# Performance work log

Hardware: AMD Instinct MI355X
Metric: run time of the kernel (lower is better)

## Reference

```python
import jax, jax.numpy as jnp
import numpy as np
import math

B, T, VOCAB, RANK = 32, 1024, 512, 256


def setup_inputs() -> dict:
    key = jax.random.key(0)
    k1, k2, k3, k4, k5 = jax.random.split(key, 5)
    scale_attn = 1.0 / math.sqrt(VOCAB)
    scale_proj = 1.0 / math.sqrt(RANK)
    return {
        "x": jax.random.normal(k1, (B, T, VOCAB), dtype=jnp.float32),
        "W_attn": jax.random.normal(k2, (VOCAB, 3 * RANK), dtype=jnp.float32) * scale_attn,
        "b_attn": jax.random.normal(k3, (3 * RANK,), dtype=jnp.float32) * 0.01,
        "W_proj": jax.random.normal(k4, (RANK, VOCAB), dtype=jnp.float32) * scale_proj,
        "b_proj": jax.random.normal(k5, (VOCAB,), dtype=jnp.float32) * 0.01,
    }


def reference(x, W_attn, b_attn, W_proj, b_proj):
    # x: [B, T, vocab]
    Bb, Tt, _ = x.shape
    qkv = x @ W_attn + b_attn              # [B, T, 3*rank]
    q, k, v = jnp.split(qkv, 3, axis=-1)   # each [B, T, rank]
    scale = 1.0 / math.sqrt(k.shape[-1])
    att = jnp.einsum('btd,bsd->bts', q, k) * scale  # [B, T, T]
    # causal mask (masked=True)
    mask = jnp.tril(jnp.ones((Tt, Tt), dtype=bool))
    att = jnp.where(mask[None, :, :], att, -jnp.inf)
    att = jax.nn.softmax(att, axis=-1)
    # dropout layers are identity in eval mode (p=0 attn, p=0.1 resid disabled)
    y = jnp.einsum('bts,bsd->btd', att, v)  # [B, T, rank]
    y = y @ W_proj + b_proj                 # [B, T, vocab]
    return jax.nn.gelu(y, approximate=False)
```

## Files before the change

### kernel.cpp

```cpp
#include <hip/hip_runtime.h>
#include <hip/hip_bf16.h>
#include <math.h>

typedef __bf16 bf16;
typedef __attribute__((ext_vector_type(8))) __bf16 bf16x8;
typedef __attribute__((ext_vector_type(4))) __bf16 bf16x4;
typedef __attribute__((ext_vector_type(4))) float f32x4;

#define MFMA16(a, b, c) __builtin_amdgcn_mfma_f32_16x16x32_bf16((a), (b), (c), 0, 0, 0)

__device__ __forceinline__ void glds16(const bf16* g, bf16* l) {
  __builtin_amdgcn_global_load_lds(
      (const __attribute__((address_space(1))) unsigned int*)g,
      (__attribute__((address_space(3))) unsigned int*)l, 16, 0, 0);
}


__global__ __launch_bounds__(256) void cvt_wattn(const float* __restrict__ w,
                                                 bf16* __restrict__ wt) {
  int o = blockIdx.x * 256 + threadIdx.x;
  int n = o >> 9, kk = o & 511;
  wt[o] = (bf16)w[kk * 768 + n];
}

__global__ __launch_bounds__(256) void cvt_wproj(const float* __restrict__ w,
                                                 bf16* __restrict__ wt) {
  int o = blockIdx.x * 256 + threadIdx.x;
  int n = o >> 8, kk = o & 255;
  wt[o] = (bf16)w[kk * 512 + n];
}

__global__ __launch_bounds__(256) void cvt_x(const float* __restrict__ x,
                                             bf16* __restrict__ xb) {
  size_t i = ((size_t)blockIdx.x * 256 + threadIdx.x) * 8;
  f32x4 f0 = *(const f32x4*)(x + i);
  f32x4 f1 = *(const f32x4*)(x + i + 4);
  bf16x8 h;
#pragma unroll
  for (int e = 0; e < 4; ++e) { h[e] = (bf16)f0[e]; h[e + 4] = (bf16)f1[e]; }
  *(bf16x8*)(xb + i) = h;
}

__global__ __launch_bounds__(256) void gemm_qkv(
    const bf16* __restrict__ xb, const bf16* __restrict__ WT,
    const float* __restrict__ b_attn,
    bf16* __restrict__ qo, bf16* __restrict__ ko, bf16* __restrict__ vo) {
  __shared__ __attribute__((aligned(16))) bf16 As[128][32];
  __shared__ __attribute__((aligned(16))) bf16 Bs[128][32];
  const int tid = threadIdx.x;
  const int id = blockIdx.x;
  const int xcd = id & 7;
  const int rest = id >> 3;
  const int bmL = rest / 6;
  const int bn = (rest % 6) * 128;
  const int bm = (xcd * 32 + bmL) * 128;
  const int lane = tid & 63, wid = tid >> 6;
  const int l15 = lane & 15, lg = lane >> 4;
  const int wm = (wid >> 1) * 64, wn = (wid & 1) * 64;

  f32x4 acc[4][4] = {};

  const int ar = tid >> 2;
  const int ac = (tid & 3) * 8;
  const bf16* aB = xb + (size_t)bm * 512 + (size_t)ar * 512 + ac;
  const bf16* bB = WT + (size_t)bn * 512 + (size_t)ar * 512 + ac;
  bf16* As0 = &As[0][0];
  bf16* Bs0 = &Bs[0][0];

  for (int kt = 0; kt < 16; ++kt) {
    const int k0 = kt * 32;
    glds16(aB + k0,            As0 + (size_t)tid * 8);
    glds16(aB + 64 * 512 + k0, As0 + (size_t)(256 + tid) * 8);
    glds16(bB + k0,            Bs0 + (size_t)tid * 8);
    glds16(bB + 64 * 512 + k0, Bs0 + (size_t)(256 + tid) * 8);
    __syncthreads();
    bf16x8 af[4], bfr[4];
#pragma unroll
    for (int mi = 0; mi < 4; ++mi)
      af[mi] = *(const bf16x8*)&As[wm + mi * 16 + l15][lg * 8];
#pragma unroll
    for (int ni = 0; ni < 4; ++ni)
      bfr[ni] = *(const bf16x8*)&Bs[wn + ni * 16 + l15][lg * 8];
#pragma unroll
    for (int mi = 0; mi < 4; ++mi)
#pragma unroll
      for (int ni = 0; ni < 4; ++ni)
        acc[mi][ni] = MFMA16(bfr[ni], af[mi], acc[mi][ni]);
    __syncthreads();
  }

#pragma unroll
  for (int ni = 0; ni < 4; ++ni) {
    int gc0 = bn + wn + ni * 16 + lg * 4;
    f32x4 bias = *(const f32x4*)(b_attn + gc0);
    int seg = gc0 >> 8;
    int cc = gc0 & 255;
    bf16* op = (seg == 0) ? qo : ((seg == 1) ? ko : vo);
#pragma unroll
    for (int mi = 0; mi < 4; ++mi) {
      int gr = bm + wm + mi * 16 + l15;
      bf16x4 pk;
#pragma unroll
      for (int r = 0; r < 4; ++r) pk[r] = (bf16)(acc[mi][ni][r] + bias[r]);
      *(bf16x4*)(op + (size_t)gr * 256 + cc) = pk;
    }
  }
}

__global__ __launch_bounds__(256) void transpose_v(const bf16* __restrict__ v,
                                                   bf16* __restrict__ vt) {
  __shared__ bf16 tile[32][33];
  const int b = blockIdx.z;
  const int t0 = blockIdx.x * 32;
  const int d0 = blockIdx.y * 32;
  const int tid = threadIdx.x;
  const int r = tid >> 3, c4 = (tid & 7) * 4;
  bf16x4 in = *(const bf16x4*)(v + (size_t)(b * 1024 + t0 + r) * 256 + d0 + c4);
  tile[r][c4] = in[0]; tile[r][c4 + 1] = in[1];
  tile[r][c4 + 2] = in[2]; tile[r][c4 + 3] = in[3];
  __syncthreads();
  bf16x4 o;
  o[0] = tile[c4][r]; o[1] = tile[c4 + 1][r];
  o[2] = tile[c4 + 2][r]; o[3] = tile[c4 + 3][r];
  *(bf16x4*)(vt + (size_t)(b * 256 + d0 + r) * 1024 + t0 + c4) = o;
}

__global__ __launch_bounds__(512) void attn_fwd(
    const bf16* __restrict__ q, const bf16* __restrict__ k,
    const bf16* __restrict__ vt, bf16* __restrict__ y) {
  __shared__ __attribute__((aligned(16))) bf16 Ks[64][264];
  __shared__ __attribute__((aligned(16))) bf16 Vt[256][72];
  __shared__ __attribute__((aligned(16))) bf16 Ps[8][16][72];
  const int tid = threadIdx.x, lane = tid & 63, wid = tid >> 6;
  const int l15 = lane & 15, lg = lane >> 4;

  const int id = blockIdx.x;
  const int xcd = id & 7;
  const int rest = id >> 3;
  const int qt = rest & 7;
  const int bg = rest >> 3;
  const int b = xcd + 8 * bg;
  const int q0 = qt * 128 + wid * 16;

  bf16x8 qf[8];
  {
    const bf16* qp = q + (size_t)(b * 1024 + q0 + l15) * 256 + lg * 8;
#pragma unroll
    for (int d = 0; d < 8; ++d) qf[d] = *(const bf16x8*)(qp + d * 32);
  }
  f32x4 o[16] = {};
  float m_st = -1e30f;
  float l_st = 0.f;

  const bf16* kbase = k + (size_t)b * 1024 * 256;
  const bf16* vtbase = vt + (size_t)b * 256 * 1024;
  const int ksr = tid >> 5, ksc = (tid & 31) * 8;
  const int vsr = tid >> 3, vsc = (tid & 7) * 8;

  const int ntiles = 2 * qt + 2;

  bf16x8 kreg[4], vreg[4];
#pragma unroll
  for (int i = 0; i < 4; ++i)
    kreg[i] = *(const bf16x8*)(kbase + (size_t)(ksr + i * 16) * 256 + ksc);
#pragma unroll
  for (int i = 0; i < 4; ++i)
    vreg[i] = *(const bf16x8*)(vtbase + (size_t)(vsr + i * 64) * 1024 + vsc);

  for (int tt = 0; tt < ntiles; ++tt) {
    const int kv0 = tt * 64;
    __syncthreads();
#pragma unroll
    for (int i = 0; i < 4; ++i)
      *(bf16x8*)&Ks[ksr + i * 16][ksc] = kreg[i];
#pragma unroll
    for (int i = 0; i < 4; ++i)
      *(bf16x8*)&Vt[vsr + i * 64][vsc] = vreg[i];
    __syncthreads();
    if (tt + 1 < ntiles) {
      const bf16* kp = kbase + (size_t)(kv0 + 64 + ksr) * 256 + ksc;
      const bf16* vp = vtbase + (size_t)vsr * 1024 + kv0 + 64 + vsc;
#pragma unroll
      for (int i = 0; i < 4; ++i)
        kreg[i] = *(const bf16x8*)(kp + (size_t)i * 16 * 256);
#pragma unroll
      for (int i = 0; i < 4; ++i)
        vreg[i] = *(const bf16x8*)(vp + (size_t)i * 64 * 1024);
    }

    f32x4 st[4] = {};
    __builtin_amdgcn_s_setprio(1);
#pragma unroll
    for (int nf = 0; nf < 4; ++nf)
#pragma unroll
      for (int dc = 0; dc < 8; ++dc) {
        bf16x8 kb = *(const bf16x8*)&Ks[nf * 16 + l15][dc * 32 + lg * 8];
        st[nf] = MFMA16(kb, qf[dc], st[nf]);
      }
    __builtin_amdgcn_s_setprio(0);

    const int qg = q0 + l15;
    float tmax = -1e30f;
#pragma unroll
    for (int nf = 0; nf < 4; ++nf)
#pragma unroll
      for (int r = 0; r < 4; ++r) {
        int sg = kv0 + nf * 16 + lg * 4 + r;
        float v = st[nf][r] * 0.0625f;
        v = (sg > qg) ? -1e30f : v;
        st[nf][r] = v;
        tmax = fmaxf(tmax, v);
      }
    tmax = fmaxf(tmax, __shfl_xor(tmax, 16, 64));
    tmax = fmaxf(tmax, __shfl_xor(tmax, 32, 64));

    if (!__all(tmax <= m_st + 8.f)) {
      float mnew = fmaxf(m_st, tmax);
      float corr = __expf(m_st - mnew);
      m_st = mnew;
      l_st *= corr;
#pragma unroll
      for (int df = 0; df < 16; ++df)
#pragma unroll
        for (int r = 0; r < 4; ++r) o[df][r] *= corr;
    }

    float rsum = 0.f;
#pragma unroll
    for (int nf = 0; nf < 4; ++nf) {
      bf16x4 pk;
#pragma unroll
      for (int r = 0; r < 4; ++r) {
        float p = __expf(st[nf][r] - m_st);
        rsum += p;
        pk[r] = (bf16)p;
      }
      *(bf16x4*)&Ps[wid][l15][nf * 16 + lg * 4] = pk;
    }
    rsum += __shfl_xor(rsum, 16, 64);
    rsum += __shfl_xor(rsum, 32, 64);
    l_st += rsum;

    bf16x8 pa0 = *(const bf16x8*)&Ps[wid][l15][lg * 8];
    bf16x8 pa1 = *(const bf16x8*)&Ps[wid][l15][32 + lg * 8];
    __builtin_amdgcn_s_setprio(1);
#pragma unroll
    for (int df = 0; df < 16; ++df) {
      bf16x8 vb0 = *(const bf16x8*)&Vt[df * 16 + l15][lg * 8];
      bf16x8 vb1 = *(const bf16x8*)&Vt[df * 16 + l15][32 + lg * 8];
      o[df] = MFMA16(vb0, pa0, o[df]);
      o[df] = MFMA16(vb1, pa1, o[df]);
    }
    __builtin_amdgcn_s_setprio(0);
  }

  float inv = 1.f / l_st;
  bf16* yp = y + (size_t)(b * 1024 + q0 + l15) * 256 + lg * 4;
#pragma unroll
  for (int df = 0; df < 16; ++df) {
    bf16x4 pk;
#pragma unroll
    for (int r = 0; r < 4; ++r) pk[r] = (bf16)(o[df][r] * inv);
    *(bf16x4*)(yp + df * 16) = pk;
  }
}

__global__ __launch_bounds__(256) void gemm_proj(
    const bf16* __restrict__ y, const bf16* __restrict__ WT,
    const float* __restrict__ b_proj, float* __restrict__ out) {
  __shared__ __attribute__((aligned(16))) bf16 As[128][32];
  __shared__ __attribute__((aligned(16))) bf16 Bs[128][32];
  const int tid = threadIdx.x;
  const int id = blockIdx.x;
  const int xcd = id & 7;
  const int rest = id >> 3;
  const int bmL = rest >> 2;
  const int bn = (rest & 3) * 128;
  const int bm = (xcd * 32 + bmL) * 128;
  const int lane = tid & 63, wid = tid >> 6;
  const int l15 = lane & 15, lg = lane >> 4;
  const int wm = (wid >> 1) * 64, wn = (wid & 1) * 64;
  f32x4 acc[4][4] = {};

  const int ar = tid >> 2;
  const int ac = (tid & 3) * 8;
  const bf16* aB = y + (size_t)bm * 256 + (size_t)ar * 256 + ac;
  const bf16* bB = WT + (size_t)bn * 256 + (size_t)ar * 256 + ac;
  bf16* As0 = &As[0][0];
  bf16* Bs0 = &Bs[0][0];

  for (int kt = 0; kt < 8; ++kt) {
    const int k0 = kt * 32;
    glds16(aB + k0,            As0 + (size_t)tid * 8);
    glds16(aB + 64 * 256 + k0, As0 + (size_t)(256 + tid) * 8);
    glds16(bB + k0,            Bs0 + (size_t)tid * 8);
    glds16(bB + 64 * 256 + k0, Bs0 + (size_t)(256 + tid) * 8);
    __syncthreads();
    bf16x8 af[4], bfr[4];
#pragma unroll
    for (int mi = 0; mi < 4; ++mi)
      af[mi] = *(const bf16x8*)&As[wm + mi * 16 + l15][lg * 8];
#pragma unroll
    for (int ni = 0; ni < 4; ++ni)
      bfr[ni] = *(const bf16x8*)&Bs[wn + ni * 16 + l15][lg * 8];
#pragma unroll
    for (int mi = 0; mi < 4; ++mi)
#pragma unroll
      for (int ni = 0; ni < 4; ++ni)
        acc[mi][ni] = MFMA16(bfr[ni], af[mi], acc[mi][ni]);
    __syncthreads();
  }

#pragma unroll
  for (int ni = 0; ni < 4; ++ni) {
    int gc0 = bn + wn + ni * 16 + lg * 4;
    f32x4 bias = *(const f32x4*)(b_proj + gc0);
#pragma unroll
    for (int mi = 0; mi < 4; ++mi) {
      int gr = bm + wm + mi * 16 + l15;
      f32x4 g;
#pragma unroll
      for (int r = 0; r < 4; ++r) {
        float v = acc[mi][ni][r] + bias[r];
        float z = 1.5957691216f * (v + 0.044715f * v * v * v);
        float t = __expf(z);
        float th = 1.f - 2.f / (t + 1.f);
        g[r] = 0.5f * v * (1.f + th);
      }
      *(f32x4*)(out + (size_t)gr * 512 + gc0) = g;
    }
  }
}

extern "C" void kernel_launch(void* const* d_in, const int* in_sizes, int n_in,
                              void* d_out, int out_size, void* d_ws, size_t ws_size,
                              hipStream_t stream) {
  const float* x      = (const float*)d_in[0];
  const float* W_attn = (const float*)d_in[1];
  const float* b_attn = (const float*)d_in[2];
  const float* W_proj = (const float*)d_in[3];
  const float* b_proj = (const float*)d_in[4];
  float* out = (float*)d_out;
  char* ws = (char*)d_ws;

  const size_t SZ = 16777216;
  bf16* WT1 = (bf16*)(ws);
  bf16* WT2 = (bf16*)(ws + 786432);
  bf16* qb  = (bf16*)(ws + 1048576);
  bf16* kb  = (bf16*)(ws + 1048576 + SZ);
  bf16* vb  = (bf16*)(ws + 1048576 + 2 * SZ);
  bf16* vtb = (bf16*)(ws + 1048576 + 3 * SZ);
  bf16* yb  = vb;
  bf16* xbb = (bf16*)(ws + 1048576 + 3 * SZ);

  cvt_wattn<<<dim3(1536), dim3(256), 0, stream>>>(W_attn, WT1);
  cvt_wproj<<<dim3(512), dim3(256), 0, stream>>>(W_proj, WT2);
  cvt_x<<<dim3(8192), dim3(256), 0, stream>>>(x, xbb);
  gemm_qkv<<<dim3(1536), dim3(256), 0, stream>>>(xbb, WT1, b_attn, qb, kb, vb);
  transpose_v<<<dim3(32, 8, 32), dim3(256), 0, stream>>>(vb, vtb);
  attn_fwd<<<dim3(256), dim3(512), 0, stream>>>(qb, kb, vtb, yb);
  gemm_proj<<<dim3(1024), dim3(256), 0, stream>>>(yb, WT2, b_proj, out);
}
```

Baseline: 162.4 us.

## Rework attention kernel with 32x32 MFMA, async LDS double buffering, swizzled tiles

Rewrites the flash-attention kernel so each of 4 waves handles 32 query rows using 32x32x16 bf16 MFMA instead of 16x16x32. K and V^T tiles are now loaded straight into double-buffered LDS with global_load_lds and an XOR swizzle, replacing the register staging and padded layout. This cuts the per-tile barriers to one and overlaps the next tile's load with compute. The cost is a larger register footprint, fewer waves per block, and a larger LDS footprint, which may reduce occupancy.

Measured after the change: 171.4 us. +5.5%, slower.

```diff
diff --git a/kernel.cpp b/kernel.cpp
--- a/kernel.cpp
+++ b/kernel.cpp
@@ -6,8 +6,10 @@
 typedef __attribute__((ext_vector_type(8))) __bf16 bf16x8;
 typedef __attribute__((ext_vector_type(4))) __bf16 bf16x4;
 typedef __attribute__((ext_vector_type(4))) float f32x4;
+typedef __attribute__((ext_vector_type(16))) float f32x16;
 
 #define MFMA16(a, b, c) __builtin_amdgcn_mfma_f32_16x16x32_bf16((a), (b), (c), 0, 0, 0)
+#define MFMA32(a, b, c) __builtin_amdgcn_mfma_f32_32x32x16_bf16((a), (b), (c), 0, 0, 0)
 
 __device__ __forceinline__ void glds16(const bf16* g, bf16* l) {
   __builtin_amdgcn_global_load_lds(
@@ -125,144 +127,156 @@
   *(bf16x4*)(vt + (size_t)(b * 256 + d0 + r) * 1024 + t0 + c4) = o;
 }
 
-__global__ __launch_bounds__(512) void attn_fwd(
+__global__ __launch_bounds__(256, 1) void attn_fwd(
     const bf16* __restrict__ q, const bf16* __restrict__ k,
     const bf16* __restrict__ vt, bf16* __restrict__ y) {
-  __shared__ __attribute__((aligned(16))) bf16 Ks[64][264];
-  __shared__ __attribute__((aligned(16))) bf16 Vt[256][72];
-  __shared__ __attribute__((aligned(16))) bf16 Ps[8][16][72];
+  __shared__ __attribute__((aligned(16))) bf16 Ks[2][64 * 256];
+  __shared__ __attribute__((aligned(16))) bf16 Vts[2][256 * 64];
+  __shared__ __attribute__((aligned(16))) bf16 Ps[4][32][68];
   const int tid = threadIdx.x, lane = tid & 63, wid = tid >> 6;
-  const int l15 = lane & 15, lg = lane >> 4;
+  const int l31 = lane & 31, hi = lane >> 5;
 
   const int id = blockIdx.x;
-  const int xcd = id & 7;
-  const int rest = id >> 3;
-  const int qt = rest & 7;
-  const int bg = rest >> 3;
+  const int xcd = id & 7, rest = id >> 3;
+  const int qt = rest & 7, bg = rest >> 3;
   const int b = xcd + 8 * bg;
-  const int q0 = qt * 128 + wid * 16;
-
-  bf16x8 qf[8];
+  const int q0 = qt * 128 + wid * 32;
+
+  bf16x8 qf[16];
   {
-    const bf16* qp = q + (size_t)(b * 1024 + q0 + l15) * 256 + lg * 8;
-#pragma unroll
-    for (int d = 0; d < 8; ++d) qf[d] = *(const bf16x8*)(qp + d * 32);
-  }
-  f32x4 o[16] = {};
+    const bf16* qp = q + (size_t)(b * 1024 + q0 + l31) * 256 + hi * 8;
+#pragma unroll
+    for (int ds = 0; ds < 16; ++ds) qf[ds] = *(const bf16x8*)(qp + ds * 16);
+  }
+  f32x16 o[8] = {};
   float m_st = -1e30f;
   float l_st = 0.f;
 
-  const bf16* kbase = k + (size_t)b * 1024 * 256;
-  const bf16* vtbase = vt + (size_t)b * 256 * 1024;
-  const int ksr = tid >> 5, ksc = (tid & 31) * 8;
-  const int vsr = tid >> 3, vsc = (tid & 7) * 8;
+  const char* kbase = (const char*)(k + (size_t)b * 1024 * 256);
+  const char* vtbase = (const char*)(vt + (size_t)b * 256 * 1024);
+  const int kr0 = tid >> 5;
+  const int ku = (tid & 31) * 16;
+  const int ksz = kr0 << 4;
+  const int vr0 = tid >> 3;
+  const int vu = (tid & 7) * 16;
+  const int vsz = (vr0 & 7) << 4;
 
   const int ntiles = 2 * qt + 2;
 
-  bf16x8 kreg[4], vreg[4];
-#pragma unroll
-  for (int i = 0; i < 4; ++i)
-    kreg[i] = *(const bf16x8*)(kbase + (size_t)(ksr + i * 16) * 256 + ksc);
-#pragma unroll
-  for (int i = 0; i < 4; ++i)
-    vreg[i] = *(const bf16x8*)(vtbase + (size_t)(vsr + i * 64) * 1024 + vsc);
-
+#pragma unroll
+  for (int i = 0; i < 8; ++i)
+    glds16((const bf16*)(kbase + (size_t)(kr0 + i * 8) * 512 + (ku ^ ksz)),
+           &Ks[0][0] + ((size_t)i * 256 + tid) * 8);
+#pragma unroll
+  for (int i = 0; i < 8; ++i)
+    glds16((const bf16*)(vtbase + (size_t)(vr0 + i * 32) * 2048 + (vu ^ vsz)),
+           &Vts[0][0] + ((size_t)i * 256 + tid) * 8);
+  __syncthreads();
+
+  int cur = 0;
   for (int tt = 0; tt < ntiles; ++tt) {
     const int kv0 = tt * 64;
-    __syncthreads();
-#pragma unroll
-    for (int i = 0; i < 4; ++i)
-      *(bf16x8*)&Ks[ksr + i * 16][ksc] = kreg[i];
-#pragma unroll
-    for (int i = 0; i < 4; ++i)
-      *(bf16x8*)&Vt[vsr + i * 64][vsc] = vreg[i];
-    __syncthreads();
     if (tt + 1 < ntiles) {
-      const bf16* kp = kbase + (size_t)(kv0 + 64 + ksr) * 256 + ksc;
-      const bf16* vp = vtbase + (size_t)vsr * 1024 + kv0 + 64 + vsc;
-#pragma unroll
-      for (int i = 0; i < 4; ++i)
-        kreg[i] = *(const bf16x8*)(kp + (size_t)i * 16 * 256);
-#pragma unroll
-      for (int i = 0; i < 4; ++i)
-        vreg[i] = *(const bf16x8*)(vp + (size_t)i * 64 * 1024);
-    }
-
-    f32x4 st[4] = {};
+      const int kvn = kv0 + 64;
+      const int nxt = cur ^ 1;
+#pragma unroll
+      for (int i = 0; i < 8; ++i)
+        glds16((const bf16*)(kbase + (size_t)(kvn + kr0 + i * 8) * 512 + (ku ^ ksz)),
+               &Ks[nxt][0] + ((size_t)i * 256 + tid) * 8);
+#pragma unroll
+      for (int i = 0; i < 8; ++i)
+        glds16((const bf16*)(vtbase + (size_t)(vr0 + i * 32) * 2048 + kvn * 2 + (vu ^ vsz)),
+               &Vts[nxt][0] + ((size_t)i * 256 + tid) * 8);
+    }
+
+    const char* kc = (const char*)&Ks[cur][0];
+    f32x16 st[2] = {};
     __builtin_amdgcn_s_setprio(1);
 #pragma unroll
-    for (int nf = 0; nf < 4; ++nf)
-#pragma unroll
-      for (int dc = 0; dc < 8; ++dc) {
-        bf16x8 kb = *(const bf16x8*)&Ks[nf * 16 + l15][dc * 32 + lg * 8];
-        st[nf] = MFMA16(kb, qf[dc], st[nf]);
-      }
+    for (int sb = 0; sb < 2; ++sb) {
+      const int row0 = sb * 32 + l31;
+      const char* rp = kc + (size_t)row0 * 512;
+      const int sw = (row0 & 7) << 4;
+#pragma unroll
+      for (int ds = 0; ds < 16; ++ds) {
+        bf16x8 kf = *(const bf16x8*)(rp + ((ds * 32 + hi * 16) ^ sw));
+        st[sb] = MFMA32(kf, qf[ds], st[sb]);
+      }
+    }
     __builtin_amdgcn_s_setprio(0);
 
-    const int qg = q0 + l15;
+    const int qg = q0 + l31;
     float tmax = -1e30f;
 #pragma unroll
-    for (int nf = 0; nf < 4; ++nf)
-#pragma unroll
-      for (int r = 0; r < 4; ++r) {
-        int sg = kv0 + nf * 16 + lg * 4 + r;
-        float v = st[nf][r] * 0.0625f;
+    for (int sb = 0; sb < 2; ++sb)
+#pragma unroll
+      for (int r = 0; r < 16; ++r) {
+        int sg = kv0 + sb * 32 + (r & 3) + 8 * (r >> 2) + 4 * hi;
+        float v = st[sb][r] * 0.0625f;
         v = (sg > qg) ? -1e30f : v;
-        st[nf][r] = v;
+        st[sb][r] = v;
         tmax = fmaxf(tmax, v);
       }
-    tmax = fmaxf(tmax, __shfl_xor(tmax, 16, 64));
     tmax = fmaxf(tmax, __shfl_xor(tmax, 32, 64));
 
     if (!__all(tmax <= m_st + 8.f)) {
       float mnew = fmaxf(m_st, tmax);
       float corr = __expf(m_st - mnew);
-      m_st = mnew;
-      l_st *= corr;
-#pragma unroll
-      for (int df = 0; df < 16; ++df)
-#pragma unroll
-        for (int r = 0; r < 4; ++r) o[df][r] *= corr;
+      m_st = mnew; l_st *= corr;
+#pragma unroll
+      for (int db = 0; db < 8; ++db)
+#pragma unroll
+        for (int r = 0; r < 16; ++r) o[db][r] *= corr;
     }
 
     float rsum = 0.f;
 #pragma unroll
-    for (int nf = 0; nf < 4; ++nf) {
-      bf16x4 pk;
-#pragma unroll
-      for (int r = 0; r < 4; ++r) {
-        float p = __expf(st[nf][r] - m_st);
-        rsum += p;
-        pk[r] = (bf16)p;
-      }
-      *(bf16x4*)&Ps[wid][l15][nf * 16 + lg * 4] = pk;
-    }
-    rsum += __shfl_xor(rsum, 16, 64);
+    for (int sb = 0; sb < 2; ++sb)
+#pragma unroll
+      for (int rb = 0; rb < 4; ++rb) {
+        bf16x4 pk;
+#pragma unroll
+        for (int j = 0; j < 4; ++j) {
+          float p = __expf(st[sb][rb * 4 + j] - m_st);
+          rsum += p;
+          pk[j] = (bf16)p;
+        }
+        *(bf16x4*)&Ps[wid][l31][sb * 32 + rb * 8 + hi * 4] = pk;
+      }
     rsum += __shfl_xor(rsum, 32, 64);
     l_st += rsum;
 
-    bf16x8 pa0 = *(const bf16x8*)&Ps[wid][l15][lg * 8];
-    bf16x8 pa1 = *(const bf16x8*)&Ps[wid][l15][32 + lg * 8];
+    const char* vc = (const char*)&Vts[cur][0];
     __builtin_amdgcn_s_setprio(1);
 #pragma unroll
-    for (int df = 0; df < 16; ++df) {
-      bf16x8 vb0 = *(const bf16x8*)&Vt[df * 16 + l15][lg * 8];
-      bf16x8 vb1 = *(const bf16x8*)&Vt[df * 16 + l15][32 + lg * 8];
-      o[df] = MFMA16(vb0, pa0, o[df]);
-      o[df] = MFMA16(vb1, pa1, o[df]);
+    for (int db = 0; db < 8; ++db) {
+      const int row0 = db * 32 + l31;
+      const char* rp = vc + (size_t)row0 * 128;
+      const int sw = (row0 & 7) << 4;
+#pragma unroll
+      for (int ss = 0; ss < 4; ++ss) {
+        bf16x8 vf = *(const bf16x8*)(rp + ((ss * 32 + hi * 16) ^ sw));
+        bf16x8 pf = *(const bf16x8*)&Ps[wid][l31][ss * 16 + hi * 8];
+        o[db] = MFMA32(vf, pf, o[db]);
+      }
     }
     __builtin_amdgcn_s_setprio(0);
+
+    __syncthreads();
+    cur ^= 1;
   }
 
   float inv = 1.f / l_st;
-  bf16* yp = y + (size_t)(b * 1024 + q0 + l15) * 256 + lg * 4;
-#pragma unroll
-  for (int df = 0; df < 16; ++df) {
-    bf16x4 pk;
-#pragma unroll
-    for (int r = 0; r < 4; ++r) pk[r] = (bf16)(o[df][r] * inv);
-    *(bf16x4*)(yp + df * 16) = pk;
-  }
+  bf16* yp = y + (size_t)(b * 1024 + q0 + l31) * 256;
+#pragma unroll
+  for (int db = 0; db < 8; ++db)
+#pragma unroll
+    for (int rb = 0; rb < 4; ++rb) {
+      bf16x4 pk;
+#pragma unroll
+      for (int j = 0; j < 4; ++j) pk[j] = (bf16)(o[db][rb * 4 + j] * inv);
+      *(bf16x4*)(yp + db * 32 + rb * 8 + hi * 4) = pk;
+    }
 }
 
 __global__ __launch_bounds__(256) void gemm_proj(
@@ -358,6 +372,6 @@
   cvt_x<<<dim3(8192), dim3(256), 0, stream>>>(x, xbb);
   gemm_qkv<<<dim3(1536), dim3(256), 0, stream>>>(xbb, WT1, b_attn, qb, kb, vb);
   transpose_v<<<dim3(32, 8, 32), dim3(256), 0, stream>>>(vb, vtb);
-  attn_fwd<<<dim3(256), dim3(512), 0, stream>>>(qb, kb, vtb, yb);
+  attn_fwd<<<dim3(256), dim3(256), 0, stream>>>(qb, kb, vtb, yb);
   gemm_proj<<<dim3(1024), dim3(256), 0, stream>>>(yb, WT2, b_proj, out);
 }
```
